# Performance work log

Hardware: AMD Instinct MI355X
Metric: run time of the kernel (lower is better)

The kernel has to match this reference:

```python
import jax, jax.numpy as jnp
import numpy as np

N = 10000       # nodes (cells)
NFEAT = 2000    # gene-expression features
NFE = 256       # embed features
NH = 128        # nhid
NHE = 64        # nhid_embed
L = 2           # gcn_hid_layers_num
NOUT = 20       # output classes
BN_EPS = 1e-5


def bn_eval(x, g, b, rm, rv):
    # BatchNorm1d in eval mode: affine with running stats
    return g * (x - rm) / jnp.sqrt(rv + BN_EPS) + b


def lstm_layer(seq, Wih, Whh, bih, bhh):
    # seq: [T, N, H_in]; PyTorch gate order i, f, g, o
    Hd = Whh.shape[1]
    def step(carry, xt):
        h, c = carry
        z = xt @ Wih.T + h @ Whh.T + bih + bhh  # [N, 4H]
        i, f, g, o = jnp.split(z, 4, axis=1)
        c = jax.nn.sigmoid(f) * c + jax.nn.sigmoid(i) * jnp.tanh(g)
        h = jax.nn.sigmoid(o) * jnp.tanh(c)
        return (h, c), h
    h0 = jnp.zeros((seq.shape[1], Hd), seq.dtype)
    _, hs = jax.lax.scan(step, (h0, h0), seq)
    return hs  # [T, N, H]


def setup_inputs() -> dict:
    key = jax.random.key(0)
    ks = iter(jax.random.split(key, 48))
    def rn(shape, scale=1.0):
        return jax.random.normal(next(ks), shape, dtype=jnp.float32) * scale
    inp = {}
    inp["x"] = rn((N, NFEAT))
    inp["embed"] = rn((N, NFE))
    inp["adj"] = jax.random.uniform(next(ks), (N, N), dtype=jnp.float32)
    inp["W_in"] = rn((NH, NFEAT), NFEAT ** -0.5); inp["b_in"] = jnp.zeros((NH,), jnp.float32)
    inp["bn_in_g"] = jnp.ones((NH,), jnp.float32); inp["bn_in_b"] = jnp.zeros((NH,), jnp.float32)
    inp["bn_in_rm"] = rn((NH,), 0.1); inp["bn_in_rv"] = jnp.ones((NH,), jnp.float32)
    # gs_block: Linear(2*nhid -> nhid) per layer (concat self + mean-aggregated neighbors)
    inp["W_gs"] = rn((L, NH, 2 * NH), (2 * NH) ** -0.5); inp["b_gs"] = jnp.zeros((L, NH), jnp.float32)
    for l in range(2):  # 2-layer LSTM jumping-knowledge
        inp[f"Wih{l}"] = rn((4 * NH, NH), NH ** -0.5)
        inp[f"Whh{l}"] = rn((4 * NH, NH), NH ** -0.5)
        inp[f"bih{l}"] = jnp.zeros((4 * NH,), jnp.float32)
        inp[f"bhh{l}"] = jnp.zeros((4 * NH,), jnp.float32)
    inp["W_emb"] = rn((NHE, NFE), NFE ** -0.5); inp["b_emb"] = jnp.zeros((NHE,), jnp.float32)
    inp["bn_emb_g"] = jnp.ones((NHE,), jnp.float32); inp["bn_emb_b"] = jnp.zeros((NHE,), jnp.float32)
    inp["bn_emb_rm"] = rn((NHE,), 0.1); inp["bn_emb_rv"] = jnp.ones((NHE,), jnp.float32)
    D = NH + NHE
    inp["W_fc"] = rn((D, D), D ** -0.5); inp["b_fc"] = jnp.zeros((D,), jnp.float32)
    inp["bn_fc_g"] = jnp.ones((D,), jnp.float32); inp["bn_fc_b"] = jnp.zeros((D,), jnp.float32)
    inp["bn_fc_rm"] = rn((D,), 0.1); inp["bn_fc_rv"] = jnp.ones((D,), jnp.float32)
    inp["W_out"] = rn((NOUT, D), D ** -0.5); inp["b_out"] = jnp.zeros((NOUT,), jnp.float32)
    return inp


def _forward(x, embed, adj, W_in, b_in, bn_in_g, bn_in_b, bn_in_rm, bn_in_rv,
             W_gs, b_gs, Wih0, Whh0, bih0, bhh0, Wih1, Whh1, bih1, bhh1,
             W_emb, b_emb, bn_emb_g, bn_emb_b, bn_emb_rm, bn_emb_rv,
             W_fc, b_fc, bn_fc_g, bn_fc_b, bn_fc_rm, bn_fc_rv, W_out, b_out):
    # input projection + BN + ELU (dropout: eval mode -> no-op)
    h = jax.nn.elu(bn_eval(x @ W_in.T + b_in, bn_in_g, bn_in_b, bn_in_rm, bn_in_rv))
    # GraphSAGE mean aggregator: row-normalized dense adjacency
    adj_norm = adj / adj.sum(1, keepdims=True)
    jk = []
    for l in range(L):
        neigh = adj_norm @ h                              # [N, NH] neighbor mean
        comb = jnp.concatenate([h, neigh], axis=1)        # [N, 2NH] (gcn=False)
        h = jax.nn.relu(comb @ W_gs[l].T + b_gs[l])
        h = h / jnp.maximum(jnp.linalg.norm(h, axis=1, keepdims=True), 1e-12)  # F.normalize
        jk.append(h)
    seq = jnp.stack(jk, 0)                                # [L, N, NH]
    hs = lstm_layer(seq, Wih0, Whh0, bih0, bhh0)
    hs = lstm_layer(hs, Wih1, Whh1, bih1, bhh1)
    h = hs.mean(0)                                        # JK: mean of LSTM outputs
    h = jax.nn.elu(bn_eval(h, bn_in_g, bn_in_b, bn_in_rm, bn_in_rv))  # bn_node_in_exp reused
    e = jax.nn.elu(bn_eval(embed @ W_emb.T + b_emb, bn_emb_g, bn_emb_b, bn_emb_rm, bn_emb_rv))
    h = jnp.concatenate([h, e], axis=1)                   # [N, NH+NHE]
    h = jax.nn.elu(bn_eval(h @ W_fc.T + b_fc, bn_fc_g, bn_fc_b, bn_fc_rm, bn_fc_rv))
    logits = h @ W_out.T + b_out
    return jax.nn.log_softmax(logits, axis=1)


def reference(x, embed, adj, W_in, b_in, bn_in_g, bn_in_b, bn_in_rm, bn_in_rv,
              W_gs, b_gs, Wih0, Whh0, bih0, bhh0, Wih1, Whh1, bih1, bhh1,
              W_emb, b_emb, bn_emb_g, bn_emb_b, bn_emb_rm, bn_emb_rv,
              W_fc, b_fc, bn_fc_g, bn_fc_b, bn_fc_rm, bn_fc_rv, W_out, b_out):
    return _forward(x, embed, adj, W_in, b_in, bn_in_g, bn_in_b, bn_in_rm, bn_in_rv,
                    W_gs, b_gs, Wih0, Whh0, bih0, bhh0, Wih1, Whh1, bih1, bhh1,
                    W_emb, b_emb, bn_emb_g, bn_emb_b, bn_emb_rm, bn_emb_rv,
                    W_fc, b_fc, bn_fc_g, bn_fc_b, bn_fc_rm, bn_fc_rv, W_out, b_out)
```

## Files before the change

kernel.cpp:

```cpp
#include <hip/hip_runtime.h>
#include <hip/hip_bf16.h>
#include <math.h>

#define N_NODES 10000
#define NFEAT   2000
#define NFE     256
#define NH      128
#define NHE     64
#define NOUT    20
#define DCAT    192
#define BN_EPS  1e-5f

#define KP      10016
#define KSTEPS  313
#define MT      157
#define NSPLIT  8
#define KC      40
#define NSPLX   4
#define MPAD    10048

typedef __attribute__((ext_vector_type(8))) short  bf16x8;
typedef __attribute__((ext_vector_type(4))) float  f32x4;

__device__ __forceinline__ float sigm(float x) { return 1.0f / (1.0f + expf(-x)); }

__device__ __forceinline__ unsigned short f2bf(float x) {
    union { __hip_bfloat16 h; unsigned short u; } c;
    c.h = __float2bfloat16(x);
    return c.u;
}

__device__ __forceinline__ bf16x8 cvt8(const float* v) {
    bf16x8 r;
    #pragma unroll
    for (int i = 0; i < 8; ++i) r[i] = (short)f2bf(v[i]);
    return r;
}

__global__ __launch_bounds__(256) void wconv_kernel(const float* __restrict__ Wih0,
                                                    const float* __restrict__ Whh0,
                                                    const float* __restrict__ Wih1,
                                                    const float* __restrict__ Whh1,
                                                    const float* __restrict__ Wgs,
                                                    unsigned short* __restrict__ wl,
                                                    unsigned short* __restrict__ wgb)
{
    const int total = 262144 + 65536;
    for (int i = blockIdx.x * 256 + threadIdx.x; i < total; i += gridDim.x * 256) {
        if (i < 262144) {
            int l = i >> 17, rem = i & 131071;
            int n = rem >> 8, k = rem & 255;
            const float* src;
            if (l == 0) src = (k < 128) ? (Wih0 + n * 128 + k) : (Whh0 + n * 128 + (k - 128));
            else        src = (k < 128) ? (Wih1 + n * 128 + k) : (Whh1 + n * 128 + (k - 128));
            wl[i] = f2bf(*src);
        } else {
            int j = i - 262144;
            wgb[j] = f2bf(Wgs[j]);
        }
    }
}

__global__ __launch_bounds__(256) void adjmm_kernel(const float* __restrict__ adj,
                                                    const unsigned short* __restrict__ hT,
                                                    float* __restrict__ part,
                                                    float* __restrict__ part_s)
{
    __shared__ unsigned short sa[64 * 32];
    __shared__ unsigned short sb[128 * 32];
    const int tid  = threadIdx.x;
    const int lane = tid & 63, w = tid >> 6;
    const int m0   = blockIdx.x * 64;
    const int ks0  = blockIdx.y * KC;
    const int ks1  = min(ks0 + KC, KSTEPS);
    const int r0   = (w & 1) * 32;
    const int c0   = (w >> 1) * 64;

    const int arow = tid >> 2, agrp = tid & 3;
    const size_t abase = (size_t)min(m0 + arow, N_NODES - 1) * N_NODES;
    const int bcol = tid >> 1, bg0 = (tid & 1) * 2;

    float rs = 0.f;
    f32x4 acc[2][4];
    #pragma unroll
    for (int i = 0; i < 2; ++i)
        #pragma unroll
        for (int j = 0; j < 4; ++j) acc[i][j] = (f32x4){0.f, 0.f, 0.f, 0.f};

    for (int ks = ks0; ks < ks1; ++ks) {
        const int k0 = ks * 32;
        const int kg = k0 + agrp * 8;
        float av8[8];
        if (kg + 8 <= N_NODES) {
            float4 u0 = *(const float4*)(adj + abase + kg);
            float4 u1 = *(const float4*)(adj + abase + kg + 4);
            av8[0] = u0.x; av8[1] = u0.y; av8[2] = u0.z; av8[3] = u0.w;
            av8[4] = u1.x; av8[5] = u1.y; av8[6] = u1.z; av8[7] = u1.w;
        } else {
            #pragma unroll
            for (int i = 0; i < 8; ++i) av8[i] = 0.f;
        }
        #pragma unroll
        for (int i = 0; i < 8; ++i) rs += av8[i];
        bf16x8 vb0 = *(const bf16x8*)(hT + (size_t)bcol * KP + k0 + bg0 * 8);
        bf16x8 vb1 = *(const bf16x8*)(hT + (size_t)bcol * KP + k0 + (bg0 + 1) * 8);
        __syncthreads();
        *(bf16x8*)(sa + arow * 32 + ((agrp ^ (arow & 3)) << 3)) = cvt8(av8);
        *(bf16x8*)(sb + bcol * 32 + (((bg0 + 0) ^ (bcol & 3)) << 3)) = vb0;
        *(bf16x8*)(sb + bcol * 32 + (((bg0 + 1) ^ (bcol & 3)) << 3)) = vb1;
        __syncthreads();
        bf16x8 av[2], bv[4];
        #pragma unroll
        for (int rb = 0; rb < 2; ++rb) {
            int row = r0 + rb * 16 + (lane & 15);
            int g   = lane >> 4;
            av[rb] = *(const bf16x8*)(sa + row * 32 + ((g ^ (row & 3)) << 3));
        }
        #pragma unroll
        for (int cb = 0; cb < 4; ++cb) {
            int col = c0 + cb * 16 + (lane & 15);
            int g   = lane >> 4;
            bv[cb] = *(const bf16x8*)(sb + col * 32 + ((g ^ (col & 3)) << 3));
        }
        #pragma unroll
        for (int rb = 0; rb < 2; ++rb)
            #pragma unroll
            for (int cb = 0; cb < 4; ++cb)
                acc[rb][cb] = __builtin_amdgcn_mfma_f32_16x16x32_bf16(av[rb], bv[cb],
                                                                      acc[rb][cb], 0, 0, 0);
    }

    rs += __shfl_xor(rs, 1);
    rs += __shfl_xor(rs, 2);
    if ((tid & 3) == 0) part_s[(size_t)blockIdx.y * MPAD + m0 + arow] = rs;

    float* pout = part + (size_t)blockIdx.y * MPAD * NH;
    #pragma unroll
    for (int rb = 0; rb < 2; ++rb)
        #pragma unroll
        for (int cb = 0; cb < 4; ++cb) {
            int rowb = m0 + r0 + rb * 16 + (lane >> 4) * 4;
            int col  = c0 + cb * 16 + (lane & 15);
            #pragma unroll
            for (int reg = 0; reg < 4; ++reg)
                pout[(size_t)(rowb + reg) * NH + col] = acc[rb][cb][reg];
        }
}

__global__ __launch_bounds__(256) void nreduce_kernel(const float* __restrict__ part,
                                                      const float* __restrict__ part_s,
                                                      float* __restrict__ neigh)
{
    int idx = blockIdx.x * 256 + threadIdx.x;
    if (idx >= N_NODES * NH / 4) return;
    const int m = idx >> 5;
    const int lane = threadIdx.x & 63;
    float inv = 0.f;
    if ((lane & 31) == 0) {
        float a = 0.f;
        #pragma unroll
        for (int c = 0; c < NSPLIT; ++c) a += part_s[(size_t)c * MPAD + m];
        inv = 1.0f / a;
    }
    inv = __shfl(inv, lane & 32);
    const size_t ch = (size_t)MPAD * NH / 4;
    const float4* p = (const float4*)part;
    float a0 = 0.f, a1 = 0.f, a2 = 0.f, a3 = 0.f;
    #pragma unroll
    for (int c = 0; c < NSPLIT; ++c) {
        float4 v = p[c * ch + idx];
        a0 += v.x; a1 += v.y; a2 += v.z; a3 += v.w;
    }
    float4 o; o.x = a0 * inv; o.y = a1 * inv; o.z = a2 * inv; o.w = a3 * inv;
    *(float4*)(neigh + (size_t)idx * 4) = o;
}

__global__ __launch_bounds__(256) void xw_mfma_kernel(const float* __restrict__ x,
                                                      const float* __restrict__ Wn,
                                                      float* __restrict__ part)
{
    __shared__ unsigned short sa[64 * 32];
    __shared__ unsigned short sb[128 * 32];
    const int tid  = threadIdx.x;
    const int lane = tid & 63, w = tid >> 6;
    const int m0   = blockIdx.x * 64;
    const int TOT  = (NFEAT + 31) / 32;
    const int s0   = blockIdx.y * 16;
    const int s1   = min(s0 + 16, TOT);
    const int r0   = (w & 1) * 32;
    const int c0   = (w >> 1) * 64;

    const int arow = tid >> 2, agrp = tid & 3;
    const size_t abase = (size_t)min(m0 + arow, N_NODES - 1) * NFEAT;

    f32x4 acc[2][4];
    #pragma unroll
    for (int i = 0; i < 2; ++i)
        #pragma unroll
        for (int j = 0; j < 4; ++j) acc[i][j] = (f32x4){0.f, 0.f, 0.f, 0.f};

    for (int ks = s0; ks < s1; ++ks) {
        const int k0 = ks * 32;
        float av8[8], bv8[2][8];
        {
            const int kg = k0 + agrp * 8;
            if (kg + 8 <= NFEAT) {
                float4 u0 = *(const float4*)(x + abase + kg);
                float4 u1 = *(const float4*)(x + abase + kg + 4);
                av8[0]=u0.x; av8[1]=u0.y; av8[2]=u0.z; av8[3]=u0.w;
                av8[4]=u1.x; av8[5]=u1.y; av8[6]=u1.z; av8[7]=u1.w;
            } else {
                #pragma unroll
                for (int i = 0; i < 8; ++i) av8[i] = 0.f;
            }
        }
        #pragma unroll
        for (int t = 0; t < 2; ++t) {
            int g = tid + t * 256;
            int n = g >> 2, grp = g & 3;
            int kg = k0 + grp * 8;
            if (kg + 8 <= NFEAT) {
                float4 u0 = *(const float4*)(Wn + (size_t)n * NFEAT + kg);
                float4 u1 = *(const float4*)(Wn + (size_t)n * NFEAT + kg + 4);
                bv8[t][0]=u0.x; bv8[t][1]=u0.y; bv8[t][2]=u0.z; bv8[t][3]=u0.w;
                bv8[t][4]=u1.x; bv8[t][5]=u1.y; bv8[t][6]=u1.z; bv8[t][7]=u1.w;
            } else {
                #pragma unroll
                for (int i = 0; i < 8; ++i) bv8[t][i] = 0.f;
            }
        }
        __syncthreads();
        *(bf16x8*)(sa + arow * 32 + ((agrp ^ (arow & 3)) << 3)) = cvt8(av8);
        #pragma unroll
        for (int t = 0; t < 2; ++t) {
            int g = tid + t * 256;
            int n = g >> 2, grp = g & 3;
            *(bf16x8*)(sb + n * 32 + ((grp ^ (n & 3)) << 3)) = cvt8(bv8[t]);
        }
        __syncthreads();
        bf16x8 av[2], bv[4];
        #pragma unroll
        for (int rb = 0; rb < 2; ++rb) {
            int row = r0 + rb * 16 + (lane & 15);
            int g   = lane >> 4;
            av[rb] = *(const bf16x8*)(sa + row * 32 + ((g ^ (row & 3)) << 3));
        }
        #pragma unroll
        for (int cb = 0; cb < 4; ++cb) {
            int col = c0 + cb * 16 + (lane & 15);
            int g   = lane >> 4;
            bv[cb] = *(const bf16x8*)(sb + col * 32 + ((g ^ (col & 3)) << 3));
        }
        #pragma unroll
        for (int rb = 0; rb < 2; ++rb)
            #pragma unroll
            for (int cb = 0; cb < 4; ++cb)
                acc[rb][cb] = __builtin_amdgcn_mfma_f32_16x16x32_bf16(av[rb], bv[cb],
                                                                      acc[rb][cb], 0, 0, 0);
    }
    float* pout = part + (size_t)blockIdx.y * MPAD * NH;
    #pragma unroll
    for (int rb = 0; rb < 2; ++rb)
        #pragma unroll
        for (int cb = 0; cb < 4; ++cb) {
            int rowb = m0 + r0 + rb * 16 + (lane >> 4) * 4;
            int col  = c0 + cb * 16 + (lane & 15);
            #pragma unroll
            for (int reg = 0; reg < 4; ++reg)
                pout[(size_t)(rowb + reg) * NH + col] = acc[rb][cb][reg];
        }
}

__global__ __launch_bounds__(256) void xw_reduce_kernel(const float* __restrict__ part,
                                                        const float* __restrict__ bias,
                                                        const float* __restrict__ g,
                                                        const float* __restrict__ bb,
                                                        const float* __restrict__ rm,
                                                        const float* __restrict__ rv,
                                                        float* __restrict__ h,
                                                        unsigned short* __restrict__ hT)
{
    __shared__ unsigned short tb[128][8];
    const int tid = threadIdx.x;
    int idx = blockIdx.x * 256 + tid;
    const int c4 = (tid & 31) * 4;
    const int lr = tid >> 5;
    const int m0g = blockIdx.x * 8;
    const size_t ch = (size_t)MPAD * NH / 4;
    const float4* p = (const float4*)part;
    float a[4] = {0.f, 0.f, 0.f, 0.f};
    #pragma unroll
    for (int c = 0; c < NSPLX; ++c) {
        float4 v = p[c * ch + idx];
        a[0] += v.x; a[1] += v.y; a[2] += v.z; a[3] += v.w;
    }
    float o[4];
    #pragma unroll
    for (int j = 0; j < 4; ++j) {
        int c = c4 + j;
        float sc = g[c] / sqrtf(rv[c] + BN_EPS);
        float t = (a[j] + bias[c] - rm[c]) * sc + bb[c];
        o[j] = t > 0.f ? t : expm1f(t);
        tb[c][lr] = f2bf(o[j]);
    }
    float4 ov; ov.x = o[0]; ov.y = o[1]; ov.z = o[2]; ov.w = o[3];
    *(float4*)(h + (size_t)idx * 4) = ov;
    __syncthreads();
    if (tid < 128) {
        ushort4 v0, v1;
        v0.x = tb[tid][0]; v0.y = tb[tid][1]; v0.z = tb[tid][2]; v0.w = tb[tid][3];
        v1.x = tb[tid][4]; v1.y = tb[tid][5]; v1.z = tb[tid][6]; v1.w = tb[tid][7];
        *(ushort4*)(hT + (size_t)tid * KP + m0g)     = v0;
        *(ushort4*)(hT + (size_t)tid * KP + m0g + 4) = v1;
        if (blockIdx.x == 0) {
            ushort4 zz; zz.x = zz.y = zz.z = zz.w = 0;
            #pragma unroll
            for (int q = 0; q < 4; ++q)
                *(ushort4*)(hT + (size_t)tid * KP + 10000 + q * 4) = zz;
        }
    }
}

template<bool WRITE_T>
__global__ __launch_bounds__(256) void gs_fused_kernel(const float* __restrict__ h,
                                                       const float* __restrict__ neigh,
                                                       const unsigned short* __restrict__ Wg,
                                                       const float* __restrict__ bg,
                                                       float* __restrict__ jk,
                                                       unsigned short* __restrict__ jkT)
{
    __shared__ unsigned short sa[64 * 32];
    __shared__ unsigned short sb[128 * 32];
    __shared__ float ssq_l[64][2];
    __shared__ unsigned short tb[WRITE_T ? 128 * 64 : 1];
    const int tid  = threadIdx.x;
    const int lane = tid & 63, w = tid >> 6;
    const int m0   = blockIdx.x * 64;
    const int r0   = (w & 1) * 32;
    const int c0   = (w >> 1) * 64;
    const int arow = tid >> 2, agrp = tid & 3;
    const int mg   = min(m0 + arow, N_NODES - 1);

    f32x4 acc[2][4];
    #pragma unroll
    for (int i = 0; i < 2; ++i)
        #pragma unroll
        for (int j = 0; j < 4; ++j) acc[i][j] = (f32x4){0.f, 0.f, 0.f, 0.f};

    for (int k0 = 0; k0 < 256; k0 += 32) {
        const int kg = k0 + agrp * 8;
        const float* asrc = (kg < 128) ? (h + (size_t)mg * NH + kg)
                                       : (neigh + (size_t)mg * NH + (kg - 128));
        float4 u0 = *(const float4*)asrc;
        float4 u1 = *(const float4*)(asrc + 4);
        float a8[8] = {u0.x, u0.y, u0.z, u0.w, u1.x, u1.y, u1.z, u1.w};
        bf16x8 b8[2];
        #pragma unroll
        for (int t = 0; t < 2; ++t) {
            int gi = tid + t * 256;
            int n = gi >> 2, grp = gi & 3;
            b8[t] = *(const bf16x8*)(Wg + (size_t)n * 256 + k0 + grp * 8);
        }
        __syncthreads();
        *(bf16x8*)(sa + arow * 32 + ((agrp ^ (arow & 3)) << 3)) = cvt8(a8);
        #pragma unroll
        for (int t = 0; t < 2; ++t) {
            int gi = tid + t * 256;
            int n = gi >> 2, grp = gi & 3;
            *(bf16x8*)(sb + n * 32 + ((grp ^ (n & 3)) << 3)) = b8[t];
        }
        __syncthreads();
        bf16x8 av[2], bv[4];
        #pragma unroll
        for (int rb = 0; rb < 2; ++rb) {
            int row = r0 + rb * 16 + (lane & 15);
            int g   = lane >> 4;
            av[rb] = *(const bf16x8*)(sa + row * 32 + ((g ^ (row & 3)) << 3));
        }
        #pragma unroll
        for (int cb = 0; cb < 4; ++cb) {
            int col = c0 + cb * 16 + (lane & 15);
            int g   = lane >> 4;
            bv[cb] = *(const bf16x8*)(sb + col * 32 + ((g ^ (col & 3)) << 3));
        }
        #pragma unroll
        for (int rb = 0; rb < 2; ++rb)
            #pragma unroll
            for (int cb = 0; cb < 4; ++cb)
                acc[rb][cb] = __builtin_amdgcn_mfma_f32_16x16x32_bf16(av[rb], bv[cb],
                                                                      acc[rb][cb], 0, 0, 0);
    }

    float vv[2][4][4];
    float ps[2][4] = {};
    #pragma unroll
    for (int rb = 0; rb < 2; ++rb)
        #pragma unroll
        for (int cb = 0; cb < 4; ++cb) {
            int colg = c0 + cb * 16 + (lane & 15);
            float b = bg[colg];
            #pragma unroll
            for (int reg = 0; reg < 4; ++reg) {
                float t = fmaxf(acc[rb][cb][reg] + b, 0.f);
                vv[rb][cb][reg] = t;
                ps[rb][reg] += t * t;
            }
        }
    #pragma unroll
    for (int msk = 1; msk < 16; msk <<= 1)
        #pragma unroll
        for (int rb = 0; rb < 2; ++rb)
            #pragma unroll
            for (int reg = 0; reg < 4; ++reg)
                ps[rb][reg] += __shfl_xor(ps[rb][reg], msk);
    if ((lane & 15) == 0) {
        #pragma unroll
        for (int rb = 0; rb < 2; ++rb)
            #pragma unroll
            for (int reg = 0; reg < 4; ++reg)
                ssq_l[r0 + rb * 16 + (lane >> 4) * 4 + reg][w >> 1] = ps[rb][reg];
    }
    __syncthreads();
    #pragma unroll
    for (int rb = 0; rb < 2; ++rb)
        #pragma unroll
        for (int reg = 0; reg < 4; ++reg) {
            int lr = r0 + rb * 16 + (lane >> 4) * 4 + reg;
            float s = ssq_l[lr][0] + ssq_l[lr][1];
            float sc = 1.0f / fmaxf(sqrtf(s), 1e-12f);
            int m = m0 + lr;
            #pragma unroll
            for (int cb = 0; cb < 4; ++cb) {
                int colg = c0 + cb * 16 + (lane & 15);
                float o = vv[rb][cb][reg] * sc;
                if (m < N_NODES) jk[(size_t)m * NH + colg] = o;
                if constexpr (WRITE_T) tb[colg * 64 + lr] = f2bf(o);
            }
        }
    if constexpr (WRITE_T) {
        __syncthreads();
        #pragma unroll
        for (int p = 0; p < 4; ++p) {
            int flat = (tid + p * 256) * 8;
            int c = flat >> 6, mo = flat & 63;
            int kglob = m0 + mo;
            if (kglob < KP) {
                unsigned short tmp[8];
                #pragma unroll
                for (int i = 0; i < 8; ++i)
                    tmp[i] = (kglob + i < N_NODES) ? tb[c * 64 + mo + i] : (unsigned short)0;
                ushort4 v0, v1;
                v0.x = tmp[0]; v0.y = tmp[1]; v0.z = tmp[2]; v0.w = tmp[3];
                v1.x = tmp[4]; v1.y = tmp[5]; v1.z = tmp[6]; v1.w = tmp[7];
                *(ushort4*)(jkT + (size_t)c * KP + kglob)     = v0;
                *(ushort4*)(jkT + (size_t)c * KP + kglob + 4) = v1;
            }
        }
    }
}

template<bool HASC, bool FINAL>
__global__ __launch_bounds__(256) void lstm_fused_kernel(
    int K, const float* __restrict__ a1, const float* __restrict__ a2,
    const unsigned short* __restrict__ wl,
    const float* __restrict__ bih, const float* __restrict__ bhh,
    const float* __restrict__ cprev,
    float* __restrict__ hout, float* __restrict__ cout,
    const float* __restrict__ hmean, const float* __restrict__ bng,
    const float* __restrict__ bnb, const float* __restrict__ bnrm,
    const float* __restrict__ bnrv, float* __restrict__ hpost)
{
    __shared__ unsigned short sa[32 * 32];
    __shared__ unsigned short sb[512 * 32];
    const int tid  = threadIdx.x;
    const int lane = tid & 63, w = tid >> 6;
    const int m0   = blockIdx.x * 32;
    const int arow = tid >> 2, agrp = tid & 3;
    const int mg   = min(m0 + arow, N_NODES - 1);

    f32x4 acc[2][8];
    #pragma unroll
    for (int i = 0; i < 2; ++i)
        #pragma unroll
        for (int j = 0; j < 8; ++j) acc[i][j] = (f32x4){0.f, 0.f, 0.f, 0.f};

    for (int k0 = 0; k0 < K; k0 += 32) {
        float a8[8];
        if (tid < 128) {
            int kg = k0 + agrp * 8;
            const float* asrc = (kg < 128) ? (a1 + (size_t)mg * NH + kg)
                                           : (a2 + (size_t)mg * NH + (kg - 128));
            float4 u0 = *(const float4*)asrc;
            float4 u1 = *(const float4*)(asrc + 4);
            a8[0]=u0.x; a8[1]=u0.y; a8[2]=u0.z; a8[3]=u0.w;
            a8[4]=u1.x; a8[5]=u1.y; a8[6]=u1.z; a8[7]=u1.w;
        }
        bf16x8 b8[8];
        #pragma unroll
        for (int t = 0; t < 8; ++t) {
            int gi = tid + t * 256;
            int n = gi >> 2, grp = gi & 3;
            b8[t] = *(const bf16x8*)(wl + (size_t)n * 256 + k0 + grp * 8);
        }
        __syncthreads();
        if (tid < 128)
            *(bf16x8*)(sa + arow * 32 + ((agrp ^ (arow & 3)) << 3)) = cvt8(a8);
        #pragma unroll
        for (int t = 0; t < 8; ++t) {
            int gi = tid + t * 256;
            int n = gi >> 2, grp = gi & 3;
            *(bf16x8*)(sb + n * 32 + ((grp ^ (n & 3)) << 3)) = b8[t];
        }
        __syncthreads();
        bf16x8 av[2];
        #pragma unroll
        for (int rb = 0; rb < 2; ++rb) {
            int row = rb * 16 + (lane & 15);
            int g   = lane >> 4;
            av[rb] = *(const bf16x8*)(sa + row * 32 + ((g ^ (row & 3)) << 3));
        }
        #pragma unroll
        for (int gate = 0; gate < 4; ++gate)
            #pragma unroll
            for (int cb = 0; cb < 2; ++cb) {
                int col = gate * 128 + w * 32 + cb * 16 + (lane & 15);
                int g   = lane >> 4;
                bf16x8 bv = *(const bf16x8*)(sb + col * 32 + ((g ^ (col & 3)) << 3));
                #pragma unroll
                for (int rb = 0; rb < 2; ++rb)
                    acc[rb][gate * 2 + cb] =
                        __builtin_amdgcn_mfma_f32_16x16x32_bf16(av[rb], bv,
                                                                acc[rb][gate * 2 + cb], 0, 0, 0);
            }
    }

    #pragma unroll
    for (int cb = 0; cb < 2; ++cb) {
        const int cg = w * 32 + cb * 16 + (lane & 15);
        const float bi = bih[0 * 128 + cg] + bhh[0 * 128 + cg];
        const float bf = bih[1 * 128 + cg] + bhh[1 * 128 + cg];
        const float bgg= bih[2 * 128 + cg] + bhh[2 * 128 + cg];
        const float bo = bih[3 * 128 + cg] + bhh[3 * 128 + cg];
        float sc = 0.f, sh = 0.f;
        if constexpr (FINAL) {
            sc = bng[cg] / sqrtf(bnrv[cg] + BN_EPS);
            sh = bnb[cg] - bnrm[cg] * sc;
        }
        #pragma unroll
        for (int rb = 0; rb < 2; ++rb) {
            #pragma unroll
            for (int reg = 0; reg < 4; ++reg) {
                int m = m0 + rb * 16 + (lane >> 4) * 4 + reg;
                if (m < N_NODES) {
                    float zi = acc[rb][0 + cb][reg] + bi;
                    float zf = acc[rb][2 + cb][reg] + bf;
                    float zg = acc[rb][4 + cb][reg] + bgg;
                    float zo = acc[rb][6 + cb][reg] + bo;
                    float cn = sigm(zi) * tanhf(zg);
                    if constexpr (HASC) cn += sigm(zf) * cprev[(size_t)m * NH + cg];
                    float hv = sigm(zo) * tanhf(cn);
                    if constexpr (FINAL) {
                        float t = 0.5f * (hmean[(size_t)m * NH + cg] + hv);
                        t = t * sc + sh;
                        hpost[(size_t)m * NH + cg] = t > 0.f ? t : expm1f(t);
                    } else {
                        hout[(size_t)m * NH + cg] = hv;
                        cout[(size_t)m * NH + cg] = cn;
                    }
                }
            }
        }
    }
}

template<int BM, int BN>
__global__ __launch_bounds__(256) void wgemm_bnelu_kernel(
    int M, int K, int kSplitA,
    const float* __restrict__ a1, int lda1,
    const float* __restrict__ a2, int lda2,
    const float* __restrict__ B, int ldb, int ncol,
    float* __restrict__ out, int ldo,
    const float* __restrict__ bias,
    const float* __restrict__ bng, const float* __restrict__ bnb,
    const float* __restrict__ bnrm, const float* __restrict__ bnrv)
{
    constexpr int WC = BN / 64;
    constexpr int WR = 4 / WC;
    static_assert(WR * WC == 4 && BM == WR * 32, "geometry");
    constexpr int NGA = BM * 4 / 256;
    constexpr int NGB = BN * 4 / 256;
    __shared__ unsigned short sa[BM * 32];
    __shared__ unsigned short sb[BN * 32];
    const int tid  = threadIdx.x;
    const int lane = tid & 63, w = tid >> 6;
    const int m0   = blockIdx.x * BM, n0 = blockIdx.y * BN;
    const int r0   = (w % WR) * 32, c0 = (w / WR) * 64;

    f32x4 acc[2][4];
    #pragma unroll
    for (int i = 0; i < 2; ++i)
        #pragma unroll
        for (int j = 0; j < 4; ++j) acc[i][j] = (f32x4){0.f, 0.f, 0.f, 0.f};

    for (int k0 = 0; k0 < K; k0 += 32) {
        float ar[NGA][8], br[NGB][8];
        #pragma unroll
        for (int t = 0; t < NGA; ++t) {
            int gi = tid + t * 256;
            int row = gi >> 2, grp = gi & 3;
            int mg = min(m0 + row, M - 1);
            int kg = k0 + grp * 8;
            const float* src = (kg < kSplitA) ? (a1 + (size_t)mg * lda1 + kg)
                                              : (a2 + (size_t)mg * lda2 + (kg - kSplitA));
            float4 u0 = *(const float4*)src;
            float4 u1 = *(const float4*)(src + 4);
            ar[t][0]=u0.x; ar[t][1]=u0.y; ar[t][2]=u0.z; ar[t][3]=u0.w;
            ar[t][4]=u1.x; ar[t][5]=u1.y; ar[t][6]=u1.z; ar[t][7]=u1.w;
        }
        #pragma unroll
        for (int t = 0; t < NGB; ++t) {
            int gi = tid + t * 256;
            int n = gi >> 2, grp = gi & 3;
            int ng = min(n0 + n, ncol - 1);
            int kg = k0 + grp * 8;
            const float* src = B + (size_t)ng * ldb + kg;
            float4 u0 = *(const float4*)src;
            float4 u1 = *(const float4*)(src + 4);
            br[t][0]=u0.x; br[t][1]=u0.y; br[t][2]=u0.z; br[t][3]=u0.w;
            br[t][4]=u1.x; br[t][5]=u1.y; br[t][6]=u1.z; br[t][7]=u1.w;
        }
        __syncthreads();
        #pragma unroll
        for (int t = 0; t < NGA; ++t) {
            int gi = tid + t * 256;
            int row = gi >> 2, grp = gi & 3;
            *(bf16x8*)(sa + row * 32 + ((grp ^ (row & 3)) << 3)) = cvt8(ar[t]);
        }
        #pragma unroll
        for (int t = 0; t < NGB; ++t) {
            int gi = tid + t * 256;
            int n = gi >> 2, grp = gi & 3;
            *(bf16x8*)(sb + n * 32 + ((grp ^ (n & 3)) << 3)) = cvt8(br[t]);
        }
        __syncthreads();
        bf16x8 av[2], bv[4];
        #pragma unroll
        for (int rb = 0; rb < 2; ++rb) {
            int row = r0 + rb * 16 + (lane & 15);
            int g   = lane >> 4;
            av[rb] = *(const bf16x8*)(sa + row * 32 + ((g ^ (row & 3)) << 3));
        }
        #pragma unroll
        for (int cb = 0; cb < 4; ++cb) {
            int col = c0 + cb * 16 + (lane & 15);
            int g   = lane >> 4;
            bv[cb] = *(const bf16x8*)(sb + col * 32 + ((g ^ (col & 3)) << 3));
        }
        #pragma unroll
        for (int rb = 0; rb < 2; ++rb)
            #pragma unroll
            for (int cb = 0; cb < 4; ++cb)
                acc[rb][cb] = __builtin_amdgcn_mfma_f32_16x16x32_bf16(av[rb], bv[cb],
                                                                      acc[rb][cb], 0, 0, 0);
    }

    #pragma unroll
    for (int cb = 0; cb < 4; ++cb) {
        const int colg = n0 + c0 + cb * 16 + (lane & 15);
        const int cc = min(colg, ncol - 1);
        float badd = bias[cc];
        float sc = bng[cc] / sqrtf(bnrv[cc] + BN_EPS);
        float sh = bnb[cc] - bnrm[cc] * sc;
        #pragma unroll
        for (int rb = 0; rb < 2; ++rb) {
            int rowb = m0 + r0 + rb * 16 + (lane >> 4) * 4;
            #pragma unroll
            for (int reg = 0; reg < 4; ++reg) {
                int m = rowb + reg;
                if (m < M && colg < ncol) {
                    float t = (acc[rb][cb][reg] + badd) * sc + sh;
                    out[(size_t)m * ldo + colg] = t > 0.f ? t : expm1f(t);
                }
            }
        }
    }
}

__global__ __launch_bounds__(256) void out_kernel(const float* __restrict__ hfc,
                                                  const float* __restrict__ W_out,
                                                  const float* __restrict__ b_out,
                                                  float* __restrict__ out)
{
    __shared__ float wl[NOUT * 193];
    __shared__ float rl[4][DCAT];
    const int tid = threadIdx.x;
    for (int i = tid; i < NOUT * DCAT; i += 256)
        wl[(i / DCAT) * 193 + (i % DCAT)] = W_out[i];
    const int w = tid >> 6, lane = tid & 63;
    const int r = blockIdx.x * 4 + w;
    for (int k = lane; k < DCAT; k += 64) rl[w][k] = hfc[(size_t)r * DCAT + k];
    __syncthreads();
    const int c = lane;
    float acc = -INFINITY;
    if (c < NOUT) {
        acc = b_out[c];
        #pragma unroll 4
        for (int k = 0; k < DCAT; ++k) acc += rl[w][k] * wl[c * 193 + k];
    }
    float mx = acc;
    #pragma unroll
    for (int msk = 16; msk >= 1; msk >>= 1) mx = fmaxf(mx, __shfl_xor(mx, msk));
    float ex = (c < NOUT) ? expf(acc - mx) : 0.f;
    float sm = ex;
    #pragma unroll
    for (int msk = 16; msk >= 1; msk >>= 1) sm += __shfl_xor(sm, msk);
    if (c < NOUT) out[(size_t)r * NOUT + c] = acc - mx - logf(sm);
}

extern "C" void kernel_launch(void* const* d_in, const int* in_sizes, int n_in,
                              void* d_out, int out_size, void* d_ws, size_t ws_size,
                              hipStream_t stream)
{
    const float* x       = (const float*)d_in[0];
    const float* embed   = (const float*)d_in[1];
    const float* adj     = (const float*)d_in[2];
    const float* W_in    = (const float*)d_in[3];
    const float* b_in    = (const float*)d_in[4];
    const float* bn_in_g = (const float*)d_in[5];
    const float* bn_in_b = (const float*)d_in[6];
    const float* bn_in_rm= (const float*)d_in[7];
    const float* bn_in_rv= (const float*)d_in[8];
    const float* W_gs    = (const float*)d_in[9];
    const float* b_gs    = (const float*)d_in[10];
    const float* Wih0    = (const float*)d_in[11];
    const float* Whh0    = (const float*)d_in[12];
    const float* bih0    = (const float*)d_in[13];
    const float* bhh0    = (const float*)d_in[14];
    const float* Wih1    = (const float*)d_in[15];
    const float* Whh1    = (const float*)d_in[16];
    const float* bih1    = (const float*)d_in[17];
    const float* bhh1    = (const float*)d_in[18];
    const float* W_emb   = (const float*)d_in[19];
    const float* b_emb   = (const float*)d_in[20];
    const float* bn_e_g  = (const float*)d_in[21];
    const float* bn_e_b  = (const float*)d_in[22];
    const float* bn_e_rm = (const float*)d_in[23];
    const float* bn_e_rv = (const float*)d_in[24];
    const float* W_fc    = (const float*)d_in[25];
    const float* b_fc    = (const float*)d_in[26];
    const float* bn_f_g  = (const float*)d_in[27];
    const float* bn_f_b  = (const float*)d_in[28];
    const float* bn_f_rm = (const float*)d_in[29];
    const float* bn_f_rv = (const float*)d_in[30];
    const float* W_out   = (const float*)d_in[31];
    const float* b_out   = (const float*)d_in[32];
    float* outp = (float*)d_out;

    const size_t HB = (size_t)N_NODES * NH * sizeof(float);
    char* wp = (char*)d_ws;
    auto carve = [&](size_t bytes) {
        void* p = (void*)wp;
        wp += (bytes + 1023) & ~(size_t)1023;
        return p;
    };
    float* part  = (float*)carve((size_t)NSPLIT * MPAD * NH * sizeof(float));
    float* part_s= (float*)carve((size_t)NSPLIT * MPAD * sizeof(float));
    float* h_in  = (float*)carve(HB);
    float* neigh = (float*)carve(HB);
    float* jk0   = (float*)carve(HB);
    float* jk1   = (float*)carve(HB);
    float* h1_0  = (float*)carve(HB);
    float* h1_1  = (float*)carve(HB);
    float* c1    = (float*)carve(HB);
    float* h2_0  = (float*)carve(HB);
    float* c2    = (float*)carve(HB);
    float* hpost = (float*)carve(HB);
    float* e     = (float*)carve((size_t)N_NODES * NHE * sizeof(float));
    float* hfc   = (float*)carve((size_t)N_NODES * DCAT * sizeof(float));
    unsigned short* hT  = (unsigned short*)carve((size_t)NH * KP * 2);
    unsigned short* wl  = (unsigned short*)carve((size_t)2 * 512 * 256 * 2);
    unsigned short* wgb = (unsigned short*)carve((size_t)2 * 128 * 256 * 2);
    if ((size_t)(wp - (char*)d_ws) > ws_size) return;

    const dim3 blk(256);

    wconv_kernel<<<320, blk, 0, stream>>>(Wih0, Whh0, Wih1, Whh1, W_gs, wl, wgb);

    xw_mfma_kernel<<<dim3(MT, NSPLX), blk, 0, stream>>>(x, W_in, part);
    xw_reduce_kernel<<<1250, blk, 0, stream>>>(part, b_in, bn_in_g, bn_in_b,
                                               bn_in_rm, bn_in_rv, h_in, hT);

    adjmm_kernel<<<dim3(MT, NSPLIT), blk, 0, stream>>>(adj, hT, part, part_s);
    nreduce_kernel<<<1250, blk, 0, stream>>>(part, part_s, neigh);
    gs_fused_kernel<true><<<MT, blk, 0, stream>>>(h_in, neigh, wgb, b_gs, jk0, hT);

    adjmm_kernel<<<dim3(MT, NSPLIT), blk, 0, stream>>>(adj, hT, part, part_s);
    nreduce_kernel<<<1250, blk, 0, stream>>>(part, part_s, neigh);
    gs_fused_kernel<false><<<MT, blk, 0, stream>>>(jk0, neigh, wgb + 128 * 256, b_gs + 128,
                                                   jk1, nullptr);

    lstm_fused_kernel<false, false><<<313, blk, 0, stream>>>(
        128, jk0, jk0, wl, bih0, bhh0, nullptr, h1_0, c1,
        nullptr, nullptr, nullptr, nullptr, nullptr, nullptr);
    lstm_fused_kernel<true, false><<<313, blk, 0, stream>>>(
        256, jk1, h1_0, wl, bih0, bhh0, c1, h1_1, c1,
        nullptr, nullptr, nullptr, nullptr, nullptr, nullptr);
    lstm_fused_kernel<false, false><<<313, blk, 0, stream>>>(
        128, h1_0, h1_0, wl + 512 * 256, bih1, bhh1, nullptr, h2_0, c2,
        nullptr, nullptr, nullptr, nullptr, nullptr, nullptr);
    lstm_fused_kernel<true, true><<<313, blk, 0, stream>>>(
        256, h1_1, h2_0, wl + 512 * 256, bih1, bhh1, c2, nullptr, nullptr,
        h2_0, bn_in_g, bn_in_b, bn_in_rm, bn_in_rv, hpost);

    wgemm_bnelu_kernel<64, 128><<<dim3(MT, 1), blk, 0, stream>>>(
        N_NODES, NFE, NFE, embed, NFE, nullptr, 0,
        W_emb, NFE, NHE, e, NHE,
        b_emb, bn_e_g, bn_e_b, bn_e_rm, bn_e_rv);

    wgemm_bnelu_kernel<64, 128><<<dim3(MT, 2), blk, 0, stream>>>(
        N_NODES, DCAT, NH, hpost, NH, e, NHE,
        W_fc, DCAT, DCAT, hfc, DCAT,
        b_fc, bn_f_g, bn_f_b, bn_f_rm, bn_f_rv);

    out_kernel<<<2500, blk, 0, stream>>>(hfc, W_out, b_out, outp);
}
```

Measured before the change: 486.2 us.

## Double-buffer LDS in adj/x GEMMs and fuse split-K reduction into gs kernel

Converts the adjmm and xw MFMA kernels to double-buffered shared memory, prefetching the next K-step into registers while the current one feeds the MFMAs, which removes one barrier per step. It also drops the separate nreduce kernel: gs_fused now sums the split-K partials and row sums itself and normalises on the fly. This saves two launches and the neigh round trip through memory. The cost is doubled LDS per block, possible occupancy loss, and each gs block rereading 8 partial slices of the neighbour half.

```diff
diff --git a/kernel.cpp b/kernel.cpp
--- a/kernel.cpp
+++ b/kernel.cpp
@@ -66,8 +66,8 @@
                                                     float* __restrict__ part,
                                                     float* __restrict__ part_s)
 {
-    __shared__ unsigned short sa[64 * 32];
-    __shared__ unsigned short sb[128 * 32];
+    __shared__ unsigned short sa[2][64 * 32];
+    __shared__ unsigned short sb[2][128 * 32];
     const int tid  = threadIdx.x;
     const int lane = tid & 63, w = tid >> 6;
     const int m0   = blockIdx.x * 64;
@@ -80,6 +80,10 @@
     const size_t abase = (size_t)min(m0 + arow, N_NODES - 1) * N_NODES;
     const int bcol = tid >> 1, bg0 = (tid & 1) * 2;
 
+    const int asoff  = arow * 32 + ((agrp ^ (arow & 3)) << 3);
+    const int bsoff0 = bcol * 32 + (((bg0 + 0) ^ (bcol & 3)) << 3);
+    const int bsoff1 = bcol * 32 + (((bg0 + 1) ^ (bcol & 3)) << 3);
+
     float rs = 0.f;
     f32x4 acc[2][4];
     #pragma unroll
@@ -87,10 +91,11 @@
         #pragma unroll
         for (int j = 0; j < 4; ++j) acc[i][j] = (f32x4){0.f, 0.f, 0.f, 0.f};
 
-    for (int ks = ks0; ks < ks1; ++ks) {
+    float av8[8];
+    bf16x8 vb0, vb1;
+    auto load_step = [&](int ks) {
         const int k0 = ks * 32;
         const int kg = k0 + agrp * 8;
-        float av8[8];
         if (kg + 8 <= N_NODES) {
             float4 u0 = *(const float4*)(adj + abase + kg);
             float4 u1 = *(const float4*)(adj + abase + kg + 4);
@@ -102,25 +107,35 @@
         }
         #pragma unroll
         for (int i = 0; i < 8; ++i) rs += av8[i];
-        bf16x8 vb0 = *(const bf16x8*)(hT + (size_t)bcol * KP + k0 + bg0 * 8);
-        bf16x8 vb1 = *(const bf16x8*)(hT + (size_t)bcol * KP + k0 + (bg0 + 1) * 8);
-        __syncthreads();
-        *(bf16x8*)(sa + arow * 32 + ((agrp ^ (arow & 3)) << 3)) = cvt8(av8);
-        *(bf16x8*)(sb + bcol * 32 + (((bg0 + 0) ^ (bcol & 3)) << 3)) = vb0;
-        *(bf16x8*)(sb + bcol * 32 + (((bg0 + 1) ^ (bcol & 3)) << 3)) = vb1;
+        vb0 = *(const bf16x8*)(hT + (size_t)bcol * KP + k0 + bg0 * 8);
+        vb1 = *(const bf16x8*)(hT + (size_t)bcol * KP + k0 + (bg0 + 1) * 8);
+    };
+    auto write_step = [&](int p) {
+        *(bf16x8*)(sa[p] + asoff)  = cvt8(av8);
+        *(bf16x8*)(sb[p] + bsoff0) = vb0;
+        *(bf16x8*)(sb[p] + bsoff1) = vb1;
+    };
+
+    load_step(ks0);
+    write_step(0);
+
+    for (int ks = ks0; ks < ks1; ++ks) {
+        const int p = (ks - ks0) & 1;
+        const bool more = (ks + 1 < ks1);
+        if (more) load_step(ks + 1);
         __syncthreads();
         bf16x8 av[2], bv[4];
         #pragma unroll
         for (int rb = 0; rb < 2; ++rb) {
             int row = r0 + rb * 16 + (lane & 15);
             int g   = lane >> 4;
-            av[rb] = *(const bf16x8*)(sa + row * 32 + ((g ^ (row & 3)) << 3));
+            av[rb] = *(const bf16x8*)(sa[p] + row * 32 + ((g ^ (row & 3)) << 3));
         }
         #pragma unroll
         for (int cb = 0; cb < 4; ++cb) {
             int col = c0 + cb * 16 + (lane & 15);
             int g   = lane >> 4;
-            bv[cb] = *(const bf16x8*)(sb + col * 32 + ((g ^ (col & 3)) << 3));
+            bv[cb] = *(const bf16x8*)(sb[p] + col * 32 + ((g ^ (col & 3)) << 3));
         }
         #pragma unroll
         for (int rb = 0; rb < 2; ++rb)
@@ -128,6 +143,7 @@
             for (int cb = 0; cb < 4; ++cb)
                 acc[rb][cb] = __builtin_amdgcn_mfma_f32_16x16x32_bf16(av[rb], bv[cb],
                                                                       acc[rb][cb], 0, 0, 0);
+        if (more) write_step(p ^ 1);
     }
 
     rs += __shfl_xor(rs, 1);
@@ -145,42 +161,14 @@
             for (int reg = 0; reg < 4; ++reg)
                 pout[(size_t)(rowb + reg) * NH + col] = acc[rb][cb][reg];
         }
-}
-
-__global__ __launch_bounds__(256) void nreduce_kernel(const float* __restrict__ part,
-                                                      const float* __restrict__ part_s,
-                                                      float* __restrict__ neigh)
-{
-    int idx = blockIdx.x * 256 + threadIdx.x;
-    if (idx >= N_NODES * NH / 4) return;
-    const int m = idx >> 5;
-    const int lane = threadIdx.x & 63;
-    float inv = 0.f;
-    if ((lane & 31) == 0) {
-        float a = 0.f;
-        #pragma unroll
-        for (int c = 0; c < NSPLIT; ++c) a += part_s[(size_t)c * MPAD + m];
-        inv = 1.0f / a;
-    }
-    inv = __shfl(inv, lane & 32);
-    const size_t ch = (size_t)MPAD * NH / 4;
-    const float4* p = (const float4*)part;
-    float a0 = 0.f, a1 = 0.f, a2 = 0.f, a3 = 0.f;
-    #pragma unroll
-    for (int c = 0; c < NSPLIT; ++c) {
-        float4 v = p[c * ch + idx];
-        a0 += v.x; a1 += v.y; a2 += v.z; a3 += v.w;
-    }
-    float4 o; o.x = a0 * inv; o.y = a1 * inv; o.z = a2 * inv; o.w = a3 * inv;
-    *(float4*)(neigh + (size_t)idx * 4) = o;
 }
 
 __global__ __launch_bounds__(256) void xw_mfma_kernel(const float* __restrict__ x,
                                                       const float* __restrict__ Wn,
                                                       float* __restrict__ part)
 {
-    __shared__ unsigned short sa[64 * 32];
-    __shared__ unsigned short sb[128 * 32];
+    __shared__ unsigned short sa[2][64 * 32];
+    __shared__ unsigned short sb[2][128 * 32];
     const int tid  = threadIdx.x;
     const int lane = tid & 63, w = tid >> 6;
     const int m0   = blockIdx.x * 64;
@@ -192,6 +180,15 @@
 
     const int arow = tid >> 2, agrp = tid & 3;
     const size_t abase = (size_t)min(m0 + arow, N_NODES - 1) * NFEAT;
+    const int asoff = arow * 32 + ((agrp ^ (arow & 3)) << 3);
+    const int bn0 = tid >> 2;
+    int bn_[2], bgrp_[2], bsoff_[2];
+    #pragma unroll
+    for (int t = 0; t < 2; ++t) {
+        int gi = tid + t * 256;
+        bn_[t] = gi >> 2; bgrp_[t] = gi & 3;
+        bsoff_[t] = bn_[t] * 32 + ((bgrp_[t] ^ (bn_[t] & 3)) << 3);
+    }
 
     f32x4 acc[2][4];
     #pragma unroll
@@ -199,9 +196,9 @@
         #pragma unroll
         for (int j = 0; j < 4; ++j) acc[i][j] = (f32x4){0.f, 0.f, 0.f, 0.f};
 
-    for (int ks = s0; ks < s1; ++ks) {
+    float av8[8], bv8[2][8];
+    auto load_step = [&](int ks) {
         const int k0 = ks * 32;
-        float av8[8], bv8[2][8];
         {
             const int kg = k0 + agrp * 8;
             if (kg + 8 <= NFEAT) {
@@ -216,12 +213,10 @@
         }
         #pragma unroll
         for (int t = 0; t < 2; ++t) {
-            int g = tid + t * 256;
-            int n = g >> 2, grp = g & 3;
-            int kg = k0 + grp * 8;
+            int kg = k0 + bgrp_[t] * 8;
             if (kg + 8 <= NFEAT) {
-                float4 u0 = *(const float4*)(Wn + (size_t)n * NFEAT + kg);
-                float4 u1 = *(const float4*)(Wn + (size_t)n * NFEAT + kg + 4);
+                float4 u0 = *(const float4*)(Wn + (size_t)bn_[t] * NFEAT + kg);
+                float4 u1 = *(const float4*)(Wn + (size_t)bn_[t] * NFEAT + kg + 4);
                 bv8[t][0]=u0.x; bv8[t][1]=u0.y; bv8[t][2]=u0.z; bv8[t][3]=u0.w;
                 bv8[t][4]=u1.x; bv8[t][5]=u1.y; bv8[t][6]=u1.z; bv8[t][7]=u1.w;
             } else {
@@ -229,27 +224,34 @@
                 for (int i = 0; i < 8; ++i) bv8[t][i] = 0.f;
             }
         }
-        __syncthreads();
-        *(bf16x8*)(sa + arow * 32 + ((agrp ^ (arow & 3)) << 3)) = cvt8(av8);
-        #pragma unroll
-        for (int t = 0; t < 2; ++t) {
-            int g = tid + t * 256;
-            int n = g >> 2, grp = g & 3;
-            *(bf16x8*)(sb + n * 32 + ((grp ^ (n & 3)) << 3)) = cvt8(bv8[t]);
-        }
+    };
+    auto write_step = [&](int p) {
+        *(bf16x8*)(sa[p] + asoff) = cvt8(av8);
+        #pragma unroll
+        for (int t = 0; t < 2; ++t)
+            *(bf16x8*)(sb[p] + bsoff_[t]) = cvt8(bv8[t]);
+    };
+
+    load_step(s0);
+    write_step(0);
+
+    for (int ks = s0; ks < s1; ++ks) {
+        const int p = (ks - s0) & 1;
+        const bool more = (ks + 1 < s1);
+        if (more) load_step(ks + 1);
         __syncthreads();
         bf16x8 av[2], bv[4];
         #pragma unroll
         for (int rb = 0; rb < 2; ++rb) {
             int row = r0 + rb * 16 + (lane & 15);
             int g   = lane >> 4;
-            av[rb] = *(const bf16x8*)(sa + row * 32 + ((g ^ (row & 3)) << 3));
+            av[rb] = *(const bf16x8*)(sa[p] + row * 32 + ((g ^ (row & 3)) << 3));
         }
         #pragma unroll
         for (int cb = 0; cb < 4; ++cb) {
             int col = c0 + cb * 16 + (lane & 15);
             int g   = lane >> 4;
-            bv[cb] = *(const bf16x8*)(sb + col * 32 + ((g ^ (col & 3)) << 3));
+            bv[cb] = *(const bf16x8*)(sb[p] + col * 32 + ((g ^ (col & 3)) << 3));
         }
         #pragma unroll
         for (int rb = 0; rb < 2; ++rb)
@@ -257,6 +259,7 @@
             for (int cb = 0; cb < 4; ++cb)
                 acc[rb][cb] = __builtin_amdgcn_mfma_f32_16x16x32_bf16(av[rb], bv[cb],
                                                                       acc[rb][cb], 0, 0, 0);
+        if (more) write_step(p ^ 1);
     }
     float* pout = part + (size_t)blockIdx.y * MPAD * NH;
     #pragma unroll
@@ -323,7 +326,8 @@
 
 template<bool WRITE_T>
 __global__ __launch_bounds__(256) void gs_fused_kernel(const float* __restrict__ h,
-                                                       const float* __restrict__ neigh,
+                                                       const float* __restrict__ part,
+                                                       const float* __restrict__ part_s,
                                                        const unsigned short* __restrict__ Wg,
                                                        const float* __restrict__ bg,
                                                        float* __restrict__ jk,
@@ -341,6 +345,14 @@
     const int arow = tid >> 2, agrp = tid & 3;
     const int mg   = min(m0 + arow, N_NODES - 1);
 
+    float inv;
+    {
+        float s = 0.f;
+        #pragma unroll
+        for (int c = 0; c < NSPLIT; ++c) s += part_s[(size_t)c * MPAD + mg];
+        inv = 1.0f / s;
+    }
+
     f32x4 acc[2][4];
     #pragma unroll
     for (int i = 0; i < 2; ++i)
@@ -349,11 +361,27 @@
 
     for (int k0 = 0; k0 < 256; k0 += 32) {
         const int kg = k0 + agrp * 8;
-        const float* asrc = (kg < 128) ? (h + (size_t)mg * NH + kg)
-                                       : (neigh + (size_t)mg * NH + (kg - 128));
-        float4 u0 = *(const float4*)asrc;
-        float4 u1 = *(const float4*)(asrc + 4);
-        float a8[8] = {u0.x, u0.y, u0.z, u0.w, u1.x, u1.y, u1.z, u1.w};
+        float a8[8];
+        if (kg < 128) {
+            const float* asrc = h + (size_t)mg * NH + kg;
+            float4 u0 = *(const float4*)asrc;
+            float4 u1 = *(const float4*)(asrc + 4);
+            a8[0]=u0.x; a8[1]=u0.y; a8[2]=u0.z; a8[3]=u0.w;
+            a8[4]=u1.x; a8[5]=u1.y; a8[6]=u1.z; a8[7]=u1.w;
+        } else {
+            const int cc = kg - 128;
+            float s0x=0,s0y=0,s0z=0,s0w=0,s1x=0,s1y=0,s1z=0,s1w=0;
+            #pragma unroll
+            for (int c = 0; c < NSPLIT; ++c) {
+                const float* pp = part + (size_t)c * MPAD * NH + (size_t)mg * NH + cc;
+                float4 v0 = *(const float4*)pp;
+                float4 v1 = *(const float4*)(pp + 4);
+                s0x+=v0.x; s0y+=v0.y; s0z+=v0.z; s0w+=v0.w;
+                s1x+=v1.x; s1y+=v1.y; s1z+=v1.z; s1w+=v1.w;
+            }
+            a8[0]=s0x*inv; a8[1]=s0y*inv; a8[2]=s0z*inv; a8[3]=s0w*inv;
+            a8[4]=s1x*inv; a8[5]=s1y*inv; a8[6]=s1z*inv; a8[7]=s1w*inv;
+        }
         bf16x8 b8[2];
         #pragma unroll
         for (int t = 0; t < 2; ++t) {
@@ -766,7 +794,6 @@
     float* part  = (float*)carve((size_t)NSPLIT * MPAD * NH * sizeof(float));
     float* part_s= (float*)carve((size_t)NSPLIT * MPAD * sizeof(float));
     float* h_in  = (float*)carve(HB);
-    float* neigh = (float*)carve(HB);
     float* jk0   = (float*)carve(HB);
     float* jk1   = (float*)carve(HB);
     float* h1_0  = (float*)carve(HB);
@@ -791,13 +818,11 @@
                                                bn_in_rm, bn_in_rv, h_in, hT);
 
     adjmm_kernel<<<dim3(MT, NSPLIT), blk, 0, stream>>>(adj, hT, part, part_s);
-    nreduce_kernel<<<1250, blk, 0, stream>>>(part, part_s, neigh);
-    gs_fused_kernel<true><<<MT, blk, 0, stream>>>(h_in, neigh, wgb, b_gs, jk0, hT);
+    gs_fused_kernel<true><<<MT, blk, 0, stream>>>(h_in, part, part_s, wgb, b_gs, jk0, hT);
 
     adjmm_kernel<<<dim3(MT, NSPLIT), blk, 0, stream>>>(adj, hT, part, part_s);
-    nreduce_kernel<<<1250, blk, 0, stream>>>(part, part_s, neigh);
-    gs_fused_kernel<false><<<MT, blk, 0, stream>>>(jk0, neigh, wgb + 128 * 256, b_gs + 128,
-                                                   jk1, nullptr);
+    gs_fused_kernel<false><<<MT, blk, 0, stream>>>(jk0, part, part_s, wgb + 128 * 256,
+                                                   b_gs + 128, jk1, nullptr);
 
     lstm_fused_kernel<false, false><<<313, blk, 0, stream>>>(
         128, jk0, jk0, wl, bih0, bhh0, nullptr, h1_0, c1,
```

New measurement: 476.9 us. About the same (-1.9%).
